# Kernel optimization log

Measured on AMD Instinct MI355X. Metric: run time of the kernel, lower is better.

Reference implementation:

```python
import jax, jax.numpy as jnp
import numpy as np
from jax import lax

D = 1024
N_EXP = 8
DD = 4 * D
BS = 8192
TRAIN_CAP = 1.0
LN_EPS = 1e-5


def setup_inputs() -> dict:
    key = jax.random.key(0)
    ks = jax.random.split(key, 8)
    s = 0.02
    return {
        "x": jax.random.normal(ks[0], (BS, D), jnp.float32),
        "Wg": jax.random.normal(ks[1], (N_EXP, D), jnp.float32) * s,
        "cp_w1": jax.random.normal(ks[2], (D, D), jnp.float32) * s,
        "cp_b1": jnp.zeros((D,), jnp.float32),
        "cp_w2": jax.random.normal(ks[3], (N_EXP, D), jnp.float32) * s,
        "cp_b2": jnp.zeros((N_EXP,), jnp.float32),
        "ln_g": jnp.ones((D,), jnp.float32),
        "ln_b": jnp.zeros((D,), jnp.float32),
        "fc1s": jax.random.normal(ks[4], (N_EXP, DD, D), jnp.float32) * s,
        "b1s": jnp.zeros((N_EXP, DD), jnp.float32),
        "fc2s": jax.random.normal(ks[5], (N_EXP, D, DD), jnp.float32) * s,
        "b2s": jnp.zeros((N_EXP, D), jnp.float32),
    }


def reference(x, Wg, cp_w1, cp_b1, cp_w2, cp_b2, ln_g, ln_b, fc1s, b1s, fc2s, b2s):
    bs, d = x.shape
    n = Wg.shape[0]
    k = int(bs * TRAIN_CAP) // n  # tokens kept per expert

    # gate scores in (0,1): (tanh(x Wg^T)+1)/2   -> [bs, n]
    scores = (jnp.tanh(x @ Wg.T) + 1.0) * 0.5

    # per-expert descending sort of tokens by score
    order = jnp.argsort(-scores, axis=0)                      # [bs, n]
    sorted_w = jnp.take_along_axis(scores, order, axis=0)     # [bs, n]
    kept_w = sorted_w[:k]                                     # [k, n]
    kept_idx = order[:k]                                      # [k, n]

    # keep mask (labels for capacity predictor)
    keep_mask = jnp.zeros((bs, n), x.dtype).at[kept_idx, jnp.arange(n)[None, :]].set(1.0)

    # capacity predictor loss (BCE with logits, x detached)
    xd = lax.stop_gradient(x)
    h = jax.nn.gelu(xd @ cp_w1.T + cp_b1, approximate=True)
    logits = h @ cp_w2.T + cp_b2                              # [bs, n]
    cap_loss = jnp.mean(jnp.logaddexp(0.0, logits) - logits * keep_mask)

    # dispatch: gather selected tokens, row-major flatten of [k, n]
    idx = kept_idx.reshape(-1)                                # [k*n]
    y = x[idx]                                                # [k*n, d]

    # LayerNorm
    mu = y.mean(-1, keepdims=True)
    var = y.var(-1, keepdims=True)
    y = (y - mu) * lax.rsqrt(var + LN_EPS) * ln_g + ln_b

    # per-expert grouped GEMMs
    y3 = y.reshape(k, n, d)
    h1 = jnp.einsum('knd,nfd->knf', y3, fc1s) + b1s[None]     # [k, n, dd]
    h1 = jax.nn.gelu(h1, approximate=True)
    y2 = jnp.einsum('knf,ndf->knd', h1, fc2s) + b2s[None]     # [k, n, d]

    # weight by gate score and scatter-add back (residual)
    y2 = y2 * kept_w[..., None]
    out = x.at[idx].add(y2.reshape(k * n, d))
    return out, cap_loss
```

## Files before the change

### kernel.cpp

```cpp
#include <hip/hip_runtime.h>


#define BS_   8192
#define D_    1024
#define DD_   4096
#define NEXP  8
#define KCAP  1024

typedef unsigned int   uint32;
typedef unsigned short u16;
typedef __bf16 bf16x8  __attribute__((ext_vector_type(8)));
typedef float  f32x4   __attribute__((ext_vector_type(4)));
typedef u16    u16x8   __attribute__((ext_vector_type(8)));
typedef u16    u16x4   __attribute__((ext_vector_type(4)));

__device__ __forceinline__ u16 f2bf(float f){
  uint32 u = __float_as_uint(f);
  u = (u + 0x7fffu + ((u >> 16) & 1u)) >> 16;
  return (u16)u;
}
__device__ __forceinline__ float bf_lo(uint32 u){ return __uint_as_float(u << 16); }
__device__ __forceinline__ float bf_hi(uint32 u){ return __uint_as_float(u & 0xffff0000u); }
__device__ __forceinline__ float gelu_tanh(float v){
  return 0.5f * v * (1.0f + tanhf(0.7978845608028654f * (v + 0.044715f * v * v * v)));
}

__global__ __launch_bounds__(64)
void gating_kernel(const float* __restrict__ x, const float* __restrict__ Wg,
                   float* __restrict__ scores, uint32* __restrict__ keep_bits)
{
  const int i    = blockIdx.x;
  const int lane = threadIdx.x;
  const float* xr = x + (size_t)i * D_ + lane * 16;
  const float4 x0 = *(const float4*)(xr +  0);
  const float4 x1 = *(const float4*)(xr +  4);
  const float4 x2 = *(const float4*)(xr +  8);
  const float4 x3 = *(const float4*)(xr + 12);
  float acc[NEXP];
  #pragma unroll
  for (int e = 0; e < NEXP; e++){
    const float* wr = Wg + e * D_ + lane * 16;
    const float4 w0 = *(const float4*)(wr +  0);
    const float4 w1 = *(const float4*)(wr +  4);
    const float4 w2 = *(const float4*)(wr +  8);
    const float4 w3 = *(const float4*)(wr + 12);
    float s = x0.x*w0.x + x0.y*w0.y + x0.z*w0.z + x0.w*w0.w;
    s += x1.x*w1.x + x1.y*w1.y + x1.z*w1.z + x1.w*w1.w;
    s += x2.x*w2.x + x2.y*w2.y + x2.z*w2.z + x2.w*w2.w;
    s += x3.x*w3.x + x3.y*w3.y + x3.z*w3.z + x3.w*w3.w;
    acc[e] = s;
  }
  #pragma unroll
  for (int e = 0; e < NEXP; e++){
    #pragma unroll
    for (int off = 32; off >= 1; off >>= 1) acc[e] += __shfl_xor(acc[e], off);
  }
  if (lane == 0){
    #pragma unroll
    for (int e = 0; e < NEXP; e++) scores[i * NEXP + e] = (tanhf(acc[e]) + 1.0f) * 0.5f;
    keep_bits[i] = 0u;
  }
}

__global__ __launch_bounds__(256)
void select_kernel(const float* __restrict__ scores, uint32* __restrict__ keep_bits,
                   int* __restrict__ counts, int* __restrict__ rowlist,
                   float* __restrict__ wlist, int* __restrict__ inv)
{
  __shared__ unsigned long long sk[2048];
  const int e = blockIdx.y;
  const int i = blockIdx.x * 256 + threadIdx.x;
  const float ms = scores[i * NEXP + e];
  const unsigned long long mk =
      ((unsigned long long)__float_as_uint(ms) << 32) | (uint32)(BS_ - 1 - i);
  int cnt = 0;
  for (int base = 0; base < BS_; base += 2048){
    #pragma unroll
    for (int u = 0; u < 8; u++){
      const int j = base + (int)threadIdx.x * 8 + u;
      const float sj = scores[j * NEXP + e];
      sk[threadIdx.x * 8 + u] =
          ((unsigned long long)__float_as_uint(sj) << 32) | (uint32)(BS_ - 1 - j);
    }
    __syncthreads();
    #pragma unroll 8
    for (int jj = 0; jj < 2048; jj++) cnt += (sk[jj] > mk) ? 1 : 0;
    __syncthreads();
  }
  if (cnt < KCAP){
    const int slot = atomicAdd(&counts[e], 1);
    rowlist[e * KCAP + slot] = i;
    wlist[e * KCAP + slot]   = ms;
    inv[i * NEXP + e]        = slot;
    atomicOr(&keep_bits[i], 1u << e);
  }
}

template<bool A_BF16, bool GELU_EP, bool OUT_BF16>
__global__ __launch_bounds__(256)
void gemm_bt(const void* __restrict__ Av, const float* __restrict__ B,
             const float* __restrict__ bias, void* __restrict__ Cv,
             int M, int N, int K,
             long long sA, long long sB, long long sBias, long long sC)
{
  __shared__ u16 smA[128 * 40];
  __shared__ u16 smB[128 * 40];
  const int z    = blockIdx.z;
  const int m0   = blockIdx.y * 128;
  const int n0   = blockIdx.x * 128;
  const int tid  = threadIdx.x;
  const int srow = tid >> 1;
  const int scol = (tid & 1) * 16;
  const int lane = tid & 63, wv = tid >> 6;
  const int l15  = lane & 15, quad = lane >> 4;
  const int moff = (wv >> 1) * 64, noff = (wv & 1) * 64;

  const float* Bp  = B + (long long)z * sB + (long long)(n0 + srow) * K + scol;
  const float* Apf = nullptr; const u16* Aph = nullptr;
  if constexpr (A_BF16) Aph = (const u16*)Av  + (long long)z * sA + (long long)(m0 + srow) * K + scol;
  else                  Apf = (const float*)Av + (long long)z * sA + (long long)(m0 + srow) * K + scol;

  f32x4 acc[4][4];
  #pragma unroll
  for (int i = 0; i < 4; i++)
    #pragma unroll
    for (int j = 0; j < 4; j++)
      acc[i][j] = (f32x4){0.f, 0.f, 0.f, 0.f};

  for (int k0 = 0; k0 < K; k0 += 32){
    if constexpr (A_BF16){
      const uint4 a0 = *(const uint4*)(Aph + k0);
      const uint4 a1 = *(const uint4*)(Aph + k0 + 8);
      *(uint4*)(&smA[srow * 40 + scol])     = a0;
      *(uint4*)(&smA[srow * 40 + scol + 8]) = a1;
    } else {
      const float4 f0 = *(const float4*)(Apf + k0);
      const float4 f1 = *(const float4*)(Apf + k0 + 4);
      const float4 f2 = *(const float4*)(Apf + k0 + 8);
      const float4 f3 = *(const float4*)(Apf + k0 + 12);
      u16x8 p0, p1;
      p0[0]=f2bf(f0.x); p0[1]=f2bf(f0.y); p0[2]=f2bf(f0.z); p0[3]=f2bf(f0.w);
      p0[4]=f2bf(f1.x); p0[5]=f2bf(f1.y); p0[6]=f2bf(f1.z); p0[7]=f2bf(f1.w);
      p1[0]=f2bf(f2.x); p1[1]=f2bf(f2.y); p1[2]=f2bf(f2.z); p1[3]=f2bf(f2.w);
      p1[4]=f2bf(f3.x); p1[5]=f2bf(f3.y); p1[6]=f2bf(f3.z); p1[7]=f2bf(f3.w);
      *(u16x8*)(&smA[srow * 40 + scol])     = p0;
      *(u16x8*)(&smA[srow * 40 + scol + 8]) = p1;
    }
    {
      const float4 f0 = *(const float4*)(Bp + k0);
      const float4 f1 = *(const float4*)(Bp + k0 + 4);
      const float4 f2 = *(const float4*)(Bp + k0 + 8);
      const float4 f3 = *(const float4*)(Bp + k0 + 12);
      u16x8 p0, p1;
      p0[0]=f2bf(f0.x); p0[1]=f2bf(f0.y); p0[2]=f2bf(f0.z); p0[3]=f2bf(f0.w);
      p0[4]=f2bf(f1.x); p0[5]=f2bf(f1.y); p0[6]=f2bf(f1.z); p0[7]=f2bf(f1.w);
      p1[0]=f2bf(f2.x); p1[1]=f2bf(f2.y); p1[2]=f2bf(f2.z); p1[3]=f2bf(f2.w);
      p1[4]=f2bf(f3.x); p1[5]=f2bf(f3.y); p1[6]=f2bf(f3.z); p1[7]=f2bf(f3.w);
      *(u16x8*)(&smB[srow * 40 + scol])     = p0;
      *(u16x8*)(&smB[srow * 40 + scol + 8]) = p1;
    }
    __syncthreads();
    bf16x8 aF[4], bF[4];
    #pragma unroll
    for (int i = 0; i < 4; i++) aF[i] = *(const bf16x8*)(&smA[(moff + i * 16 + l15) * 40 + quad * 8]);
    #pragma unroll
    for (int j = 0; j < 4; j++) bF[j] = *(const bf16x8*)(&smB[(noff + j * 16 + l15) * 40 + quad * 8]);
    #pragma unroll
    for (int i = 0; i < 4; i++)
      #pragma unroll
      for (int j = 0; j < 4; j++)
        acc[i][j] = __builtin_amdgcn_mfma_f32_16x16x32_bf16(aF[i], bF[j], acc[i][j], 0, 0, 0);
    __syncthreads();
  }

  const float* biasp = bias + (long long)z * sBias;
  const long long cbase = (long long)z * sC;
  #pragma unroll
  for (int j = 0; j < 4; j++){
    const int gn = n0 + noff + j * 16 + l15;
    const float bv = biasp[gn];
    #pragma unroll
    for (int i = 0; i < 4; i++){
      const int gmb = m0 + moff + i * 16 + quad * 4;
      #pragma unroll
      for (int r = 0; r < 4; r++){
        float v = acc[i][j][r] + bv;
        if constexpr (GELU_EP) v = gelu_tanh(v);
        const long long off = cbase + (long long)(gmb + r) * N + gn;
        if constexpr (OUT_BF16) ((u16*)Cv)[off] = f2bf(v);
        else                    ((float*)Cv)[off] = v;
      }
    }
  }
}

__global__ __launch_bounds__(256)
void loss_kernel(const u16* __restrict__ h, const float* __restrict__ cp_w2,
                 const float* __restrict__ cp_b2, const uint32* __restrict__ keep_bits,
                 float* __restrict__ loss)
{
  __shared__ float bl;
  if (threadIdx.x == 0) bl = 0.f;
  __syncthreads();
  const int wv = threadIdx.x >> 6, lane = threadIdx.x & 63;
  const int i  = blockIdx.x * 4 + wv;
  const u16* hr = h + (size_t)i * D_ + lane * 16;
  const uint4 ha = *(const uint4*)(hr);
  const uint4 hb = *(const uint4*)(hr + 8);
  float hx[16];
  hx[0]=bf_lo(ha.x); hx[1]=bf_hi(ha.x); hx[2]=bf_lo(ha.y); hx[3]=bf_hi(ha.y);
  hx[4]=bf_lo(ha.z); hx[5]=bf_hi(ha.z); hx[6]=bf_lo(ha.w); hx[7]=bf_hi(ha.w);
  hx[8]=bf_lo(hb.x); hx[9]=bf_hi(hb.x); hx[10]=bf_lo(hb.y); hx[11]=bf_hi(hb.y);
  hx[12]=bf_lo(hb.z); hx[13]=bf_hi(hb.z); hx[14]=bf_lo(hb.w); hx[15]=bf_hi(hb.w);
  float acc[NEXP];
  #pragma unroll
  for (int e = 0; e < NEXP; e++){
    const float* wr = cp_w2 + e * D_ + lane * 16;
    const float4 w0 = *(const float4*)(wr +  0);
    const float4 w1 = *(const float4*)(wr +  4);
    const float4 w2 = *(const float4*)(wr +  8);
    const float4 w3 = *(const float4*)(wr + 12);
    float s = hx[0]*w0.x + hx[1]*w0.y + hx[2]*w0.z + hx[3]*w0.w;
    s += hx[4]*w1.x + hx[5]*w1.y + hx[6]*w1.z + hx[7]*w1.w;
    s += hx[8]*w2.x + hx[9]*w2.y + hx[10]*w2.z + hx[11]*w2.w;
    s += hx[12]*w3.x + hx[13]*w3.y + hx[14]*w3.z + hx[15]*w3.w;
    acc[e] = s;
  }
  #pragma unroll
  for (int e = 0; e < NEXP; e++){
    #pragma unroll
    for (int off = 32; off >= 1; off >>= 1) acc[e] += __shfl_xor(acc[e], off);
  }
  if (lane == 0){
    const uint32 kb = keep_bits[i];
    float li = 0.f;
    #pragma unroll
    for (int e = 0; e < NEXP; e++){
      const float l  = acc[e] + cp_b2[e];
      const float sp = fmaxf(l, 0.f) + log1pf(expf(-fabsf(l)));
      li += sp - l * (float)((kb >> e) & 1u);
    }
    atomicAdd(&bl, li);
  }
  __syncthreads();
  if (threadIdx.x == 0) atomicAdd(loss, bl);
}

__global__ __launch_bounds__(256)
void ln_gather_kernel(const float* __restrict__ x, const int* __restrict__ rowlist,
                      const float* __restrict__ ln_g, const float* __restrict__ ln_b,
                      u16* __restrict__ Y)
{
  __shared__ float red[8];
  const int b   = blockIdx.x;
  const int row = rowlist[b];
  const int tid = threadIdx.x;
  const float4 v = *(const float4*)(x + (size_t)row * D_ + tid * 4);
  float s = v.x + v.y + v.z + v.w;
  float q = v.x*v.x + v.y*v.y + v.z*v.z + v.w*v.w;
  const int lane = tid & 63, wv = tid >> 6;
  #pragma unroll
  for (int off = 32; off >= 1; off >>= 1){ s += __shfl_xor(s, off); q += __shfl_xor(q, off); }
  if (lane == 0){ red[wv] = s; red[4 + wv] = q; }
  __syncthreads();
  s = red[0] + red[1] + red[2] + red[3];
  q = red[4] + red[5] + red[6] + red[7];
  const float mu  = s * (1.0f / D_);
  const float var = q * (1.0f / D_) - mu * mu;
  const float rs  = rsqrtf(var + 1e-5f);
  const float4 g  = *(const float4*)(ln_g + tid * 4);
  const float4 bb = *(const float4*)(ln_b + tid * 4);
  u16x4 o;
  o[0] = f2bf((v.x - mu) * rs * g.x + bb.x);
  o[1] = f2bf((v.y - mu) * rs * g.y + bb.y);
  o[2] = f2bf((v.z - mu) * rs * g.z + bb.z);
  o[3] = f2bf((v.w - mu) * rs * g.w + bb.w);
  *(u16x4*)(&Y[(size_t)b * D_ + tid * 4]) = o;
}

__global__ __launch_bounds__(256)
void combine_kernel(const float* __restrict__ x, const uint32* __restrict__ keep_bits,
                    const int* __restrict__ inv, const float* __restrict__ wlist,
                    const float* __restrict__ Y2, float* __restrict__ out)
{
  const int i = blockIdx.x;
  const int c = threadIdx.x * 4;
  float4 v = *(const float4*)(x + (size_t)i * D_ + c);
  uint32 kb = keep_bits[i];
  while (kb){
    const int e = __ffs(kb) - 1;
    kb &= kb - 1;
    const int r = inv[i * NEXP + e];
    const float w = wlist[e * KCAP + r];
    const float4 y = *(const float4*)(Y2 + ((size_t)(e * KCAP + r)) * D_ + c);
    v.x += w * y.x; v.y += w * y.y; v.z += w * y.z; v.w += w * y.w;
  }
  *(float4*)(out + (size_t)i * D_ + c) = v;
}

__global__ void finalize_loss_kernel(const float* __restrict__ loss, float* __restrict__ outp){
  outp[0] = loss[0] * (1.0f / (float)(BS_ * NEXP));
}

extern "C" void kernel_launch(void* const* d_in, const int* in_sizes, int n_in,
                              void* d_out, int out_size, void* d_ws, size_t ws_size,
                              hipStream_t stream)
{
  const float* x     = (const float*)d_in[0];
  const float* Wg    = (const float*)d_in[1];
  const float* cp_w1 = (const float*)d_in[2];
  const float* cp_b1 = (const float*)d_in[3];
  const float* cp_w2 = (const float*)d_in[4];
  const float* cp_b2 = (const float*)d_in[5];
  const float* ln_g  = (const float*)d_in[6];
  const float* ln_b  = (const float*)d_in[7];
  const float* fc1s  = (const float*)d_in[8];
  const float* b1s   = (const float*)d_in[9];
  const float* fc2s  = (const float*)d_in[10];
  const float* b2s   = (const float*)d_in[11];
  float* out = (float*)d_out;

  char* p = (char*)d_ws;
  auto take = [&](size_t bytes) -> char* {
    char* r = p; p += (bytes + 255) & ~(size_t)255; return r;
  };
  float*  scores    = (float*) take((size_t)BS_ * NEXP * 4);
  int*    counts    = (int*)   take(256);
  float*  loss      = (float*) take(256);
  int*    rowlist   = (int*)   take((size_t)BS_ * 4);
  float*  wlist     = (float*) take((size_t)BS_ * 4);
  uint32* keep_bits = (uint32*)take((size_t)BS_ * 4);
  int*    inv       = (int*)   take((size_t)BS_ * NEXP * 4);
  u16*    h_cp      = (u16*)   take((size_t)BS_ * D_ * 2);
  u16*    Y         = (u16*)   take((size_t)NEXP * KCAP * D_ * 2);
  u16*    H1        = (u16*)   take((size_t)NEXP * KCAP * DD_ * 2);
  float*  Y2        = (float*) take((size_t)NEXP * KCAP * D_ * 4);

  hipMemsetAsync(counts, 0, 512, stream);

  gating_kernel<<<BS_, 64, 0, stream>>>(x, Wg, scores, keep_bits);

  select_kernel<<<dim3(BS_ / 256, NEXP), 256, 0, stream>>>(
      scores, keep_bits, counts, rowlist, wlist, inv);

  gemm_bt<false, true, true><<<dim3(D_ / 128, BS_ / 128, 1), 256, 0, stream>>>(
      x, cp_w1, cp_b1, h_cp, BS_, D_, D_, 0, 0, 0, 0);

  loss_kernel<<<BS_ / 4, 256, 0, stream>>>(h_cp, cp_w2, cp_b2, keep_bits, loss);

  ln_gather_kernel<<<BS_, 256, 0, stream>>>(x, rowlist, ln_g, ln_b, Y);

  gemm_bt<true, true, true><<<dim3(DD_ / 128, KCAP / 128, NEXP), 256, 0, stream>>>(
      Y, fc1s, b1s, H1, KCAP, DD_, D_,
      (long long)KCAP * D_, (long long)DD_ * D_, DD_, (long long)KCAP * DD_);

  gemm_bt<true, false, false><<<dim3(D_ / 128, KCAP / 128, NEXP), 256, 0, stream>>>(
      H1, fc2s, b2s, Y2, KCAP, D_, DD_,
      (long long)KCAP * DD_, (long long)D_ * DD_, D_, (long long)KCAP * D_);

  combine_kernel<<<BS_, 256, 0, stream>>>(x, keep_bits, inv, wlist, Y2, out);

  finalize_loss_kernel<<<1, 1, 0, stream>>>(loss, out + (size_t)BS_ * D_);
}
```

Measured before the change: 876.6 us.

## Pre-convert GEMM operands to bf16 and stream tiles into LDS directly

```diff
diff --git a/kernel.cpp b/kernel.cpp
--- a/kernel.cpp
+++ b/kernel.cpp
@@ -24,10 +24,30 @@
 __device__ __forceinline__ float gelu_tanh(float v){
   return 0.5f * v * (1.0f + tanhf(0.7978845608028654f * (v + 0.044715f * v * v * v)));
 }
+__device__ __forceinline__ void glds16(const u16* g, u16* l){
+  __builtin_amdgcn_global_load_lds(
+      (const __attribute__((address_space(1))) unsigned int*)g,
+      (__attribute__((address_space(3))) unsigned int*)l, 16, 0, 0);
+}
+
+__global__ __launch_bounds__(256)
+void convert_kernel(const float* __restrict__ in, u16* __restrict__ out, int n)
+{
+  const int stride = gridDim.x * 256 * 8;
+  for (int idx = (blockIdx.x * 256 + threadIdx.x) * 8; idx < n; idx += stride){
+    const float4 a = *(const float4*)(in + idx);
+    const float4 b = *(const float4*)(in + idx + 4);
+    u16x8 o;
+    o[0]=f2bf(a.x); o[1]=f2bf(a.y); o[2]=f2bf(a.z); o[3]=f2bf(a.w);
+    o[4]=f2bf(b.x); o[5]=f2bf(b.y); o[6]=f2bf(b.z); o[7]=f2bf(b.w);
+    *(u16x8*)(out + idx) = o;
+  }
+}
 
 __global__ __launch_bounds__(64)
 void gating_kernel(const float* __restrict__ x, const float* __restrict__ Wg,
-                   float* __restrict__ scores, uint32* __restrict__ keep_bits)
+                   float* __restrict__ scores, uint32* __restrict__ keep_bits,
+                   u16* __restrict__ xh)
 {
   const int i    = blockIdx.x;
   const int lane = threadIdx.x;
@@ -36,6 +56,14 @@
   const float4 x1 = *(const float4*)(xr +  4);
   const float4 x2 = *(const float4*)(xr +  8);
   const float4 x3 = *(const float4*)(xr + 12);
+  u16x8 p0, p1;
+  p0[0]=f2bf(x0.x); p0[1]=f2bf(x0.y); p0[2]=f2bf(x0.z); p0[3]=f2bf(x0.w);
+  p0[4]=f2bf(x1.x); p0[5]=f2bf(x1.y); p0[6]=f2bf(x1.z); p0[7]=f2bf(x1.w);
+  p1[0]=f2bf(x2.x); p1[1]=f2bf(x2.y); p1[2]=f2bf(x2.z); p1[3]=f2bf(x2.w);
+  p1[4]=f2bf(x3.x); p1[5]=f2bf(x3.y); p1[6]=f2bf(x3.z); p1[7]=f2bf(x3.w);
+  *(u16x8*)(xh + (size_t)i * D_ + lane * 16)     = p0;
+  *(u16x8*)(xh + (size_t)i * D_ + lane * 16 + 8) = p1;
+
   float acc[NEXP];
   #pragma unroll
   for (int e = 0; e < NEXP; e++){
@@ -96,29 +124,29 @@
   }
 }
 
-template<bool A_BF16, bool GELU_EP, bool OUT_BF16>
-__global__ __launch_bounds__(256)
-void gemm_bt(const void* __restrict__ Av, const float* __restrict__ B,
-             const float* __restrict__ bias, void* __restrict__ Cv,
-             int M, int N, int K,
-             long long sA, long long sB, long long sBias, long long sC)
-{
-  __shared__ u16 smA[128 * 40];
-  __shared__ u16 smB[128 * 40];
+template<bool GELU_EP, bool OUT_BF16>
+__global__ __launch_bounds__(256)
+void gemm_bt16(const u16* __restrict__ A, const u16* __restrict__ B,
+               const float* __restrict__ bias, void* __restrict__ Cv,
+               int M, int N, int K,
+               long long sA, long long sB, long long sBias, long long sC)
+{
+  __shared__ u16 smA[128 * 32];
+  __shared__ u16 smB[128 * 32];
   const int z    = blockIdx.z;
   const int m0   = blockIdx.y * 128;
   const int n0   = blockIdx.x * 128;
   const int tid  = threadIdx.x;
-  const int srow = tid >> 1;
-  const int scol = (tid & 1) * 16;
   const int lane = tid & 63, wv = tid >> 6;
   const int l15  = lane & 15, quad = lane >> 4;
   const int moff = (wv >> 1) * 64, noff = (wv & 1) * 64;
 
-  const float* Bp  = B + (long long)z * sB + (long long)(n0 + srow) * K + scol;
-  const float* Apf = nullptr; const u16* Aph = nullptr;
-  if constexpr (A_BF16) Aph = (const u16*)Av  + (long long)z * sA + (long long)(m0 + srow) * K + scol;
-  else                  Apf = (const float*)Av + (long long)z * sA + (long long)(m0 + srow) * K + scol;
+  const int srow = wv * 32 + (lane >> 2);
+  const int skol = (lane & 3) * 8;
+  const u16* Ag = A + (long long)z * sA + (long long)(m0 + srow) * K + skol;
+  const u16* Bg = B + (long long)z * sB + (long long)(n0 + srow) * K + skol;
+  u16* lA = smA + wv * 1024;
+  u16* lB = smB + wv * 1024;
 
   f32x4 acc[4][4];
   #pragma unroll
@@ -128,43 +156,19 @@
       acc[i][j] = (f32x4){0.f, 0.f, 0.f, 0.f};
 
   for (int k0 = 0; k0 < K; k0 += 32){
-    if constexpr (A_BF16){
-      const uint4 a0 = *(const uint4*)(Aph + k0);
-      const uint4 a1 = *(const uint4*)(Aph + k0 + 8);
-      *(uint4*)(&smA[srow * 40 + scol])     = a0;
-      *(uint4*)(&smA[srow * 40 + scol + 8]) = a1;
-    } else {
-      const float4 f0 = *(const float4*)(Apf + k0);
-      const float4 f1 = *(const float4*)(Apf + k0 + 4);
-      const float4 f2 = *(const float4*)(Apf + k0 + 8);
-      const float4 f3 = *(const float4*)(Apf + k0 + 12);
-      u16x8 p0, p1;
-      p0[0]=f2bf(f0.x); p0[1]=f2bf(f0.y); p0[2]=f2bf(f0.z); p0[3]=f2bf(f0.w);
-      p0[4]=f2bf(f1.x); p0[5]=f2bf(f1.y); p0[6]=f2bf(f1.z); p0[7]=f2bf(f1.w);
-      p1[0]=f2bf(f2.x); p1[1]=f2bf(f2.y); p1[2]=f2bf(f2.z); p1[3]=f2bf(f2.w);
-      p1[4]=f2bf(f3.x); p1[5]=f2bf(f3.y); p1[6]=f2bf(f3.z); p1[7]=f2bf(f3.w);
-      *(u16x8*)(&smA[srow * 40 + scol])     = p0;
-      *(u16x8*)(&smA[srow * 40 + scol + 8]) = p1;
-    }
-    {
-      const float4 f0 = *(const float4*)(Bp + k0);
-      const float4 f1 = *(const float4*)(Bp + k0 + 4);
-      const float4 f2 = *(const float4*)(Bp + k0 + 8);
-      const float4 f3 = *(const float4*)(Bp + k0 + 12);
-      u16x8 p0, p1;
-      p0[0]=f2bf(f0.x); p0[1]=f2bf(f0.y); p0[2]=f2bf(f0.z); p0[3]=f2bf(f0.w);
-      p0[4]=f2bf(f1.x); p0[5]=f2bf(f1.y); p0[6]=f2bf(f1.z); p0[7]=f2bf(f1.w);
-      p1[0]=f2bf(f2.x); p1[1]=f2bf(f2.y); p1[2]=f2bf(f2.z); p1[3]=f2bf(f2.w);
-      p1[4]=f2bf(f3.x); p1[5]=f2bf(f3.y); p1[6]=f2bf(f3.z); p1[7]=f2bf(f3.w);
-      *(u16x8*)(&smB[srow * 40 + scol])     = p0;
-      *(u16x8*)(&smB[srow * 40 + scol + 8]) = p1;
+    #pragma unroll
+    for (int c = 0; c < 2; c++){
+      glds16(Ag + (long long)(c * 16) * K + k0, lA + c * 512);
+      glds16(Bg + (long long)(c * 16) * K + k0, lB + c * 512);
     }
     __syncthreads();
     bf16x8 aF[4], bF[4];
     #pragma unroll
-    for (int i = 0; i < 4; i++) aF[i] = *(const bf16x8*)(&smA[(moff + i * 16 + l15) * 40 + quad * 8]);
-    #pragma unroll
-    for (int j = 0; j < 4; j++) bF[j] = *(const bf16x8*)(&smB[(noff + j * 16 + l15) * 40 + quad * 8]);
+    for (int i = 0; i < 4; i++)
+      aF[i] = *(const bf16x8*)(smA + (moff + i * 16 + l15) * 32 + quad * 8);
+    #pragma unroll
+    for (int j = 0; j < 4; j++)
+      bF[j] = *(const bf16x8*)(smB + (noff + j * 16 + l15) * 32 + quad * 8);
     #pragma unroll
     for (int i = 0; i < 4; i++)
       #pragma unroll
@@ -331,31 +335,39 @@
   float*  wlist     = (float*) take((size_t)BS_ * 4);
   uint32* keep_bits = (uint32*)take((size_t)BS_ * 4);
   int*    inv       = (int*)   take((size_t)BS_ * NEXP * 4);
+  u16*    xh        = (u16*)   take((size_t)BS_ * D_ * 2);
+  u16*    cpw1h     = (u16*)   take((size_t)D_ * D_ * 2);
+  u16*    fc1h      = (u16*)   take((size_t)NEXP * DD_ * D_ * 2);
+  u16*    fc2h      = (u16*)   take((size_t)NEXP * D_ * DD_ * 2);
+  u16*    H1        = (u16*)   take((size_t)NEXP * KCAP * DD_ * 2);
   u16*    h_cp      = (u16*)   take((size_t)BS_ * D_ * 2);
   u16*    Y         = (u16*)   take((size_t)NEXP * KCAP * D_ * 2);
-  u16*    H1        = (u16*)   take((size_t)NEXP * KCAP * DD_ * 2);
-  float*  Y2        = (float*) take((size_t)NEXP * KCAP * D_ * 4);
+  float*  Y2        = (float*)h_cp;
 
   hipMemsetAsync(counts, 0, 512, stream);
 
-  gating_kernel<<<BS_, 64, 0, stream>>>(x, Wg, scores, keep_bits);
+  convert_kernel<<<512,  256, 0, stream>>>(cp_w1, cpw1h, D_ * D_);
+  convert_kernel<<<8192, 256, 0, stream>>>(fc1s, fc1h, NEXP * DD_ * D_);
+  convert_kernel<<<8192, 256, 0, stream>>>(fc2s, fc2h, NEXP * D_ * DD_);
+
+  gating_kernel<<<BS_, 64, 0, stream>>>(x, Wg, scores, keep_bits, xh);
 
   select_kernel<<<dim3(BS_ / 256, NEXP), 256, 0, stream>>>(
       scores, keep_bits, counts, rowlist, wlist, inv);
 
-  gemm_bt<false, true, true><<<dim3(D_ / 128, BS_ / 128, 1), 256, 0, stream>>>(
-      x, cp_w1, cp_b1, h_cp, BS_, D_, D_, 0, 0, 0, 0);
+  gemm_bt16<true, true><<<dim3(D_ / 128, BS_ / 128, 1), 256, 0, stream>>>(
+      xh, cpw1h, cp_b1, h_cp, BS_, D_, D_, 0, 0, 0, 0);
 
   loss_kernel<<<BS_ / 4, 256, 0, stream>>>(h_cp, cp_w2, cp_b2, keep_bits, loss);
 
   ln_gather_kernel<<<BS_, 256, 0, stream>>>(x, rowlist, ln_g, ln_b, Y);
 
-  gemm_bt<true, true, true><<<dim3(DD_ / 128, KCAP / 128, NEXP), 256, 0, stream>>>(
-      Y, fc1s, b1s, H1, KCAP, DD_, D_,
+  gemm_bt16<true, true><<<dim3(DD_ / 128, KCAP / 128, NEXP), 256, 0, stream>>>(
+      Y, fc1h, b1s, H1, KCAP, DD_, D_,
       (long long)KCAP * D_, (long long)DD_ * D_, DD_, (long long)KCAP * DD_);
 
-  gemm_bt<true, false, false><<<dim3(D_ / 128, KCAP / 128, NEXP), 256, 0, stream>>>(
-      H1, fc2s, b2s, Y2, KCAP, D_, DD_,
+  gemm_bt16<false, false><<<dim3(D_ / 128, KCAP / 128, NEXP), 256, 0, stream>>>(
+      H1, fc2h, b2s, Y2, KCAP, D_, DD_,
       (long long)KCAP * DD_, (long long)D_ * DD_, D_, (long long)KCAP * D_);
 
   combine_kernel<<<BS_, 256, 0, stream>>>(x, keep_bits, inv, wlist, Y2, out);
```

Measured after the change: 871.3 us. Within noise of the previous version (-0.6%).
